# Performance work log

Measured on AMD Instinct MI355X. Metric: run time of the kernel, lower is better.

## Reference

```python
import jax, jax.numpy as jnp
import numpy as np

B, T, D, H = 8, 1024, 1024, 16
DH = D // H  # head dim = 64


def setup_inputs() -> dict:
    key = jax.random.key(0)
    ks = jax.random.split(key, 16)
    std_qk = np.sqrt(2.0 / (D + DH)).astype(np.float32)
    inp = {
        "query": jax.random.normal(ks[0], (B, T, D), jnp.float32),
        "key": jax.random.normal(ks[1], (B, T, D), jnp.float32),
        "value": jax.random.normal(ks[2], (B, T, D), jnp.float32),
        "spatial_encoding": jax.random.normal(ks[3], (B, T, T), jnp.float32),
        "edge_encoding": jax.random.normal(ks[4], (B, T, T), jnp.float32),
        "key_padding_mask": jax.random.bernoulli(ks[5], 0.1, (B, T)),  # True = masked key
        # Linear params stored as (in, out); y = x @ W + b (equivalent to torch x @ W.T + b)
        "Wq": jax.random.normal(ks[6], (D, D), jnp.float32) * std_qk,
        "bq": jnp.zeros((D,), jnp.float32),
        "Wk": jax.random.normal(ks[7], (D, D), jnp.float32) * std_qk,
        "bk": jnp.zeros((D,), jnp.float32),
        "Wv": jax.random.normal(ks[8], (D, D), jnp.float32) * std_qk,
        "bv": jnp.zeros((D,), jnp.float32),
        "Wo": jax.random.normal(ks[9], (D, D), jnp.float32),
        "bo": jnp.zeros((D,), jnp.float32),
    }
    return inp


def reference(query, key, value, spatial_encoding, edge_encoding, key_padding_mask,
              Wq, bq, Wk, bk, Wv, bv, Wo, bo):
    # QKV projections -> (B, H, T, DH)
    def proj(x, W, b):
        return (x @ W + b).reshape(B, T, H, DH).transpose(0, 2, 1, 3)

    q = proj(query, Wq, bq)
    k = proj(key, Wk, bk)
    v = proj(value, Wv, bv)

    # attention bias: spatial + edge, masked by key padding (broadcast over heads)
    attn_bias = (spatial_encoding + edge_encoding)[:, None, :, :]  # (B,1,T,T)
    neg_inf = jnp.float32(-jnp.inf)
    attn_bias = jnp.where(key_padding_mask[:, None, None, :], neg_inf, attn_bias)

    scale = 1.0 / np.sqrt(DH).astype(np.float32)
    scores = jnp.einsum('bhqd,bhkd->bhqk', q, k) * scale + attn_bias  # (B,H,T,T)
    attn = jax.nn.softmax(scores, axis=-1)
    out = jnp.einsum('bhqk,bhkd->bhqd', attn, v)  # (B,H,T,DH)
    out = out.transpose(0, 2, 1, 3).reshape(B, T, D)
    return out @ Wo + bo
```

## Files before the change

### kernel.cpp

```cpp
#include <hip/hip_runtime.h>
#include <hip/hip_bf16.h>

#define BB 8
#define TT 1024
#define DD 1024
#define HH 16
#define DH 64
#define QKVLD 3072

typedef __attribute__((ext_vector_type(8))) short short8;
typedef __attribute__((ext_vector_type(4))) float f32x4;

__device__ __forceinline__ unsigned short f2bf(float f) {
  unsigned int u = __builtin_bit_cast(unsigned int, f);
  unsigned int rounding = 0x7fffu + ((u >> 16) & 1u);
  u += rounding;
  return (unsigned short)(u >> 16);
}

__device__ __forceinline__ void gload16(const void* g, void* l) {
  __builtin_amdgcn_global_load_lds((const __attribute__((address_space(1))) void*)g,
                                   (__attribute__((address_space(3))) void*)l, 16, 0, 0);
}

__global__ __launch_bounds__(256) void convertT4_k(const float* __restrict__ w0,
                                                   const float* __restrict__ w1,
                                                   const float* __restrict__ w2,
                                                   const float* __restrict__ w3,
                                                   unsigned short* __restrict__ out) {
  int bx = blockIdx.x;
  int seg = bx >> 9;
  const float* in = seg == 0 ? w0 : seg == 1 ? w1 : seg == 2 ? w2 : w3;
  unsigned short* o = out + (size_t)seg * DD * DD;
  int g = (bx & 511) * 256 + threadIdx.x;
  int n = g & (DD - 1);
  int kb = (g >> 10) * 8;
  short8 v;
#pragma unroll
  for (int j = 0; j < 8; ++j) v[j] = (short)f2bf(in[(size_t)(kb + j) * DD + n]);
  *(short8*)(o + (size_t)n * DD + kb) = v;
}

__global__ __launch_bounds__(256) void gemm_qkv_k(const float* __restrict__ Aq,
                                                  const float* __restrict__ Ak,
                                                  const float* __restrict__ Av,
                                                  const unsigned short* __restrict__ Wt3,
                                                  const float* __restrict__ bq,
                                                  const float* __restrict__ bk,
                                                  const float* __restrict__ bv,
                                                  unsigned short* __restrict__ C) {
  __shared__ unsigned short Bs[128 * 64];
  __shared__ unsigned short As[128 * 72];
  const int tid = threadIdx.x, lane = tid & 63, w = tid >> 6;
  const int lo = lane & 15, hi = lane >> 4;
  const int wm = w >> 1, wn = w & 1;
  const int seg = blockIdx.x >> 3;
  const float* Ap = seg == 0 ? Aq : seg == 1 ? Ak : Av;
  const float* bias = seg == 0 ? bq : seg == 1 ? bk : bv;
  const int n0 = blockIdx.x * 128;
  const int m0 = blockIdx.y * 128;
  f32x4 acc[4][4] = {};
  int dmn[4], dmk[4];
#pragma unroll
  for (int i = 0; i < 4; ++i) {
    int d = i * 4096 + w * 1024 + lane * 16;
    int lz = d ^ (((d >> 7) & 7) << 4);
    dmn[i] = d >> 7;
    dmk[i] = (lz & 127) >> 1;
  }
  for (int k0 = 0; k0 < DD; k0 += 64) {
#pragma unroll
    for (int i = 0; i < 4; ++i)
      gload16(Wt3 + (size_t)(n0 + dmn[i]) * DD + k0 + dmk[i], &Bs[(i * 4096 + w * 1024) >> 1]);
#pragma unroll
    for (int it = 0; it < 4; ++it) {
      int c = tid + 256 * it;
      int r = c >> 3, cb = (c & 7) * 8;
      const float* src = Ap + (size_t)(m0 + r) * DD + k0 + cb;
      float4 v0 = *(const float4*)src;
      float4 v1 = *(const float4*)(src + 4);
      short8 sv;
      sv[0] = (short)f2bf(v0.x); sv[1] = (short)f2bf(v0.y);
      sv[2] = (short)f2bf(v0.z); sv[3] = (short)f2bf(v0.w);
      sv[4] = (short)f2bf(v1.x); sv[5] = (short)f2bf(v1.y);
      sv[6] = (short)f2bf(v1.z); sv[7] = (short)f2bf(v1.w);
      *(short8*)&As[r * 72 + cb] = sv;
    }
    __syncthreads();
#pragma unroll
    for (int s = 0; s < 2; ++s) {
      short8 af[4], bf[4];
#pragma unroll
      for (int mt = 0; mt < 4; ++mt)
        af[mt] = *(const short8*)&As[(wm * 64 + mt * 16 + lo) * 72 + s * 32 + hi * 8];
#pragma unroll
      for (int nt = 0; nt < 4; ++nt) {
        int nr = wn * 64 + nt * 16 + lo;
        int byte = (nr * 128 + s * 64 + hi * 16) ^ ((nr & 7) << 4);
        bf[nt] = *(const short8*)((const char*)Bs + byte);
      }
#pragma unroll
      for (int mt = 0; mt < 4; ++mt)
#pragma unroll
        for (int nt = 0; nt < 4; ++nt)
          acc[mt][nt] = __builtin_amdgcn_mfma_f32_16x16x32_bf16(af[mt], bf[nt], acc[mt][nt], 0, 0, 0);
    }
    __syncthreads();
  }
#pragma unroll
  for (int mt = 0; mt < 4; ++mt)
#pragma unroll
    for (int nt = 0; nt < 4; ++nt) {
      int cl = wn * 64 + nt * 16 + lo;
      float bvv = bias[(n0 & 1023) + cl];
      int col = n0 + cl;
#pragma unroll
      for (int r = 0; r < 4; ++r) {
        int row = m0 + wm * 64 + mt * 16 + hi * 4 + r;
        C[(size_t)row * QKVLD + col] = f2bf(acc[mt][nt][r] + bvv);
      }
    }
}

__global__ __launch_bounds__(256) void gemm_out_k(const unsigned short* __restrict__ Aobf,
                                                  const unsigned short* __restrict__ WoT,
                                                  const float* __restrict__ bo,
                                                  float* __restrict__ out) {
  __shared__ unsigned short Bs[128 * 64];
  __shared__ unsigned short As[128 * 64];
  const int tid = threadIdx.x, lane = tid & 63, w = tid >> 6;
  const int lo = lane & 15, hi = lane >> 4;
  const int wm = w >> 1, wn = w & 1;
  const int n0 = blockIdx.x * 128;
  const int m0 = blockIdx.y * 128;
  f32x4 acc[4][4] = {};
  int dmn[4], dmk[4];
#pragma unroll
  for (int i = 0; i < 4; ++i) {
    int d = i * 4096 + w * 1024 + lane * 16;
    int lz = d ^ (((d >> 7) & 7) << 4);
    dmn[i] = d >> 7;
    dmk[i] = (lz & 127) >> 1;
  }
  for (int k0 = 0; k0 < DD; k0 += 64) {
#pragma unroll
    for (int i = 0; i < 4; ++i) {
      gload16(WoT + (size_t)(n0 + dmn[i]) * DD + k0 + dmk[i], &Bs[(i * 4096 + w * 1024) >> 1]);
      gload16(Aobf + (size_t)(m0 + dmn[i]) * DD + k0 + dmk[i], &As[(i * 4096 + w * 1024) >> 1]);
    }
    __syncthreads();
#pragma unroll
    for (int s = 0; s < 2; ++s) {
      short8 af[4], bf[4];
#pragma unroll
      for (int mt = 0; mt < 4; ++mt) {
        int mr = wm * 64 + mt * 16 + lo;
        int byte = (mr * 128 + s * 64 + hi * 16) ^ ((mr & 7) << 4);
        af[mt] = *(const short8*)((const char*)As + byte);
      }
#pragma unroll
      for (int nt = 0; nt < 4; ++nt) {
        int nr = wn * 64 + nt * 16 + lo;
        int byte = (nr * 128 + s * 64 + hi * 16) ^ ((nr & 7) << 4);
        bf[nt] = *(const short8*)((const char*)Bs + byte);
      }
#pragma unroll
      for (int mt = 0; mt < 4; ++mt)
#pragma unroll
        for (int nt = 0; nt < 4; ++nt)
          acc[mt][nt] = __builtin_amdgcn_mfma_f32_16x16x32_bf16(af[mt], bf[nt], acc[mt][nt], 0, 0, 0);
    }
    __syncthreads();
  }
#pragma unroll
  for (int mt = 0; mt < 4; ++mt)
#pragma unroll
    for (int nt = 0; nt < 4; ++nt) {
      int col = n0 + wn * 64 + nt * 16 + lo;
      float bvv = bo[col];
#pragma unroll
      for (int r = 0; r < 4; ++r) {
        int row = m0 + wm * 64 + mt * 16 + hi * 4 + r;
        out[(size_t)row * DD + col] = acc[mt][nt][r] + bvv;
      }
    }
}

__global__ __launch_bounds__(256) void transpose_v_k(const unsigned short* __restrict__ QKV,
                                                     unsigned short* __restrict__ Vt) {
  __shared__ unsigned short tile[64][72];
  const int blk = blockIdx.x;
  const int t0 = (blk & 15) * 64;
  const int h = (blk >> 4) & 15;
  const int b = blk >> 8;
  const int tid = threadIdx.x;
#pragma unroll
  for (int it = 0; it < 2; ++it) {
    int c = tid + 256 * it;
    int r = c >> 3, d8 = (c & 7) * 8;
    short8 v = *(const short8*)(QKV + ((size_t)(b * TT + t0 + r)) * QKVLD + 2048 + h * DH + d8);
    *(short8*)&tile[r][d8] = v;
  }
  __syncthreads();
#pragma unroll
  for (int it = 0; it < 2; ++it) {
    int c = tid + 256 * it;
    int d = c >> 3, t8 = (c & 7) * 8;
    short8 o;
#pragma unroll
    for (int j = 0; j < 8; ++j) o[j] = (short)tile[t8 + j][d];
    *(short8*)(Vt + ((size_t)(b * HH + h) * DH + d) * TT + t0 + t8) = o;
  }
}

__global__ __launch_bounds__(256) void attn_k(const unsigned short* __restrict__ QKV,
                                              const unsigned short* __restrict__ Vt,
                                              const float* __restrict__ spat,
                                              const float* __restrict__ edge,
                                              const int* __restrict__ mask,
                                              unsigned short* __restrict__ Obf) {
  __shared__ unsigned short P[4][16][72];
  const int blk = blockIdx.x;
  const int qt = blk & 15;
  const int h = (blk >> 4) & 15;
  const int b = blk >> 8;
  const int tid = threadIdx.x;
  const int w = tid >> 6;
  const int lane = tid & 63;
  const int lo = lane & 15, hi = lane >> 4;
  const int q0 = qt * 64 + w * 16;

  const unsigned short* Qb = QKV + ((size_t)(b * TT + q0)) * QKVLD + h * DH;
  const unsigned short* Kb = QKV + (size_t)b * TT * QKVLD + 1024 + h * DH;
  const unsigned short* Vb = Vt + (size_t)(b * HH + h) * DH * TT;
  const float* Sp = spat + (size_t)b * TT * TT;
  const float* Ed = edge + (size_t)b * TT * TT;
  const int* Mk = mask + b * TT;

  short8 qf0 = *(const short8*)(Qb + (size_t)lo * QKVLD + hi * 8);
  short8 qf1 = *(const short8*)(Qb + (size_t)lo * QKVLD + 32 + hi * 8);

  float m[4], l[4];
  f32x4 acc[4] = {};
#pragma unroll
  for (int r = 0; r < 4; ++r) { m[r] = -INFINITY; l[r] = 0.f; }

  for (int k0 = 0; k0 < TT; k0 += 64) {
    short8 kf[8];
#pragma unroll
    for (int kt = 0; kt < 4; ++kt) {
      const unsigned short* kp = Kb + (size_t)(k0 + kt * 16 + lo) * QKVLD + hi * 8;
      kf[kt * 2] = *(const short8*)kp;
      kf[kt * 2 + 1] = *(const short8*)(kp + 32);
    }
    int mk[4];
#pragma unroll
    for (int kt = 0; kt < 4; ++kt) mk[kt] = Mk[k0 + kt * 16 + lo];

    f32x4 sc[4];
#pragma unroll
    for (int kt = 0; kt < 4; ++kt) {
      f32x4 z = {};
      z = __builtin_amdgcn_mfma_f32_16x16x32_bf16(qf0, kf[kt * 2], z, 0, 0, 0);
      sc[kt] = __builtin_amdgcn_mfma_f32_16x16x32_bf16(qf1, kf[kt * 2 + 1], z, 0, 0, 0);
    }

    float alpha[4];
#pragma unroll
    for (int r = 0; r < 4; ++r) {
      const size_t roff = (size_t)(q0 + hi * 4 + r) * TT + k0;
      const float* srow = Sp + roff;
      const float* erow = Ed + roff;
      float s[4];
#pragma unroll
      for (int j = 0; j < 4; ++j) {
        float bb = mk[j] ? -1e30f : (srow[j * 16 + lo] + erow[j * 16 + lo]);
        s[j] = sc[j][r] * 0.125f + bb;
      }
      float mx = fmaxf(fmaxf(s[0], s[1]), fmaxf(s[2], s[3]));
      mx = fmaxf(mx, __shfl_xor(mx, 1));
      mx = fmaxf(mx, __shfl_xor(mx, 2));
      mx = fmaxf(mx, __shfl_xor(mx, 4));
      mx = fmaxf(mx, __shfl_xor(mx, 8));
      float mn = fmaxf(m[r], mx);
      alpha[r] = __expf(m[r] - mn);
      m[r] = mn;
      float rs = 0.f;
#pragma unroll
      for (int j = 0; j < 4; ++j) {
        s[j] = __expf(s[j] - mn);
        rs += s[j];
        P[w][hi * 4 + r][j * 16 + lo] = f2bf(s[j]);
      }
      rs += __shfl_xor(rs, 1);
      rs += __shfl_xor(rs, 2);
      rs += __shfl_xor(rs, 4);
      rs += __shfl_xor(rs, 8);
      l[r] = l[r] * alpha[r] + rs;
    }
#pragma unroll
    for (int dt = 0; dt < 4; ++dt)
#pragma unroll
      for (int r = 0; r < 4; ++r) acc[dt][r] *= alpha[r];

#pragma unroll
    for (int kc = 0; kc < 2; ++kc) {
      short8 pf = *(const short8*)&P[w][lo][kc * 32 + hi * 8];
#pragma unroll
      for (int dt = 0; dt < 4; ++dt) {
        short8 vf = *(const short8*)(Vb + (size_t)(dt * 16 + lo) * TT + k0 + kc * 32 + hi * 8);
        acc[dt] = __builtin_amdgcn_mfma_f32_16x16x32_bf16(pf, vf, acc[dt], 0, 0, 0);
      }
    }
  }

  float rl[4];
#pragma unroll
  for (int r = 0; r < 4; ++r) rl[r] = 1.0f / l[r];
  unsigned short* Ob = Obf + ((size_t)b * TT + q0) * DD + h * DH;
#pragma unroll
  for (int dt = 0; dt < 4; ++dt)
#pragma unroll
    for (int r = 0; r < 4; ++r)
      Ob[(size_t)(hi * 4 + r) * DD + dt * 16 + lo] = f2bf(acc[dt][r] * rl[r]);
}

extern "C" void kernel_launch(void* const* d_in, const int* in_sizes, int n_in,
                              void* d_out, int out_size, void* d_ws, size_t ws_size,
                              hipStream_t stream) {
  const float* query = (const float*)d_in[0];
  const float* key   = (const float*)d_in[1];
  const float* value = (const float*)d_in[2];
  const float* spat  = (const float*)d_in[3];
  const float* edge  = (const float*)d_in[4];
  const int*   maskp = (const int*)d_in[5];
  const float* Wq = (const float*)d_in[6];  const float* bq = (const float*)d_in[7];
  const float* Wk = (const float*)d_in[8];  const float* bk = (const float*)d_in[9];
  const float* Wv = (const float*)d_in[10]; const float* bv = (const float*)d_in[11];
  const float* Wo = (const float*)d_in[12]; const float* bo = (const float*)d_in[13];
  float* out = (float*)d_out;

  const int M = BB * TT;
  unsigned short* WT3 = (unsigned short*)d_ws;
  unsigned short* WoT = WT3 + (size_t)3 * DD * DD;
  unsigned short* QKV = WoT + (size_t)DD * DD;
  unsigned short* Vt  = QKV + (size_t)M * QKVLD;
  unsigned short* Obf = Vt + (size_t)M * DD;

  convertT4_k<<<2048, 256, 0, stream>>>(Wq, Wk, Wv, Wo, WT3);

  gemm_qkv_k<<<dim3(24, M / 128), 256, 0, stream>>>(query, key, value, WT3, bq, bk, bv, QKV);

  transpose_v_k<<<BB * HH * (TT / 64), 256, 0, stream>>>(QKV, Vt);

  attn_k<<<BB * HH * (TT / 64), 256, 0, stream>>>(QKV, Vt, spat, edge, maskp, Obf);

  gemm_out_k<<<dim3(DD / 128, M / 128), 256, 0, stream>>>(Obf, WoT, bo, out);
}
```

Baseline: 746.4 us.

## Double-buffer bias tiles into LDS via async global loads in attention

The spatial and edge bias tiles are now prefetched one key block ahead into a double-buffered shared-memory area using direct global-to-LDS loads. The goal is to overlap the large fp32 bias reads with the MFMA and softmax work, instead of issuing scattered per-lane global loads inside the loop. The 1/sqrt(d) scale is also folded into Q once in bf16, which removes a multiply per score but rounds Q again. This adds 64KB of LDS per block, which may cut occupancy, and a block-wide barrier on every iteration.

```diff
diff --git a/kernel.cpp b/kernel.cpp
--- a/kernel.cpp
+++ b/kernel.cpp
@@ -16,6 +16,10 @@
   unsigned int rounding = 0x7fffu + ((u >> 16) & 1u);
   u += rounding;
   return (unsigned short)(u >> 16);
+}
+__device__ __forceinline__ float bf2f(unsigned short u) {
+  unsigned int x = ((unsigned int)u) << 16;
+  return __builtin_bit_cast(float, x);
 }
 
 __device__ __forceinline__ void gload16(const void* g, void* l) {
@@ -219,6 +223,7 @@
                                               const float* __restrict__ edge,
                                               const int* __restrict__ mask,
                                               unsigned short* __restrict__ Obf) {
+  __shared__ float SB[2][2][4][16][64];
   __shared__ unsigned short P[4][16][72];
   const int blk = blockIdx.x;
   const int qt = blk & 15;
@@ -233,19 +238,42 @@
   const unsigned short* Qb = QKV + ((size_t)(b * TT + q0)) * QKVLD + h * DH;
   const unsigned short* Kb = QKV + (size_t)b * TT * QKVLD + 1024 + h * DH;
   const unsigned short* Vb = Vt + (size_t)(b * HH + h) * DH * TT;
-  const float* Sp = spat + (size_t)b * TT * TT;
-  const float* Ed = edge + (size_t)b * TT * TT;
   const int* Mk = mask + b * TT;
-
-  short8 qf0 = *(const short8*)(Qb + (size_t)lo * QKVLD + hi * 8);
-  short8 qf1 = *(const short8*)(Qb + (size_t)lo * QKVLD + 32 + hi * 8);
+  const float* SpW = spat + (size_t)b * TT * TT + (size_t)(q0 + (lane >> 4)) * TT + (lane & 15) * 4;
+  const float* EdW = edge + (size_t)b * TT * TT + (size_t)(q0 + (lane >> 4)) * TT + (lane & 15) * 4;
+
+#define STAGE(bf, kk)                                              \
+  do {                                                             \
+    _Pragma("unroll") for (int i_ = 0; i_ < 4; ++i_) {             \
+      gload16(SpW + (size_t)i_ * 4 * TT + (kk), &SB[bf][0][w][i_ * 4][0]); \
+      gload16(EdW + (size_t)i_ * 4 * TT + (kk), &SB[bf][1][w][i_ * 4][0]); \
+    }                                                              \
+  } while (0)
+
+  short8 qf0, qf1;
+  {
+    short8 qr0 = *(const short8*)(Qb + (size_t)lo * QKVLD + hi * 8);
+    short8 qr1 = *(const short8*)(Qb + (size_t)lo * QKVLD + 32 + hi * 8);
+#pragma unroll
+    for (int j = 0; j < 8; ++j) {
+      qf0[j] = (short)f2bf(bf2f((unsigned short)qr0[j]) * 0.125f);
+      qf1[j] = (short)f2bf(bf2f((unsigned short)qr1[j]) * 0.125f);
+    }
+  }
 
   float m[4], l[4];
   f32x4 acc[4] = {};
 #pragma unroll
   for (int r = 0; r < 4; ++r) { m[r] = -INFINITY; l[r] = 0.f; }
 
-  for (int k0 = 0; k0 < TT; k0 += 64) {
+  STAGE(0, 0);
+  __syncthreads();
+
+  for (int t = 0; t < 16; ++t) {
+    const int k0 = t * 64;
+    const int cur = t & 1;
+    if (t < 15) STAGE(cur ^ 1, k0 + 64);
+
     short8 kf[8];
 #pragma unroll
     for (int kt = 0; kt < 4; ++kt) {
@@ -268,14 +296,13 @@
     float alpha[4];
 #pragma unroll
     for (int r = 0; r < 4; ++r) {
-      const size_t roff = (size_t)(q0 + hi * 4 + r) * TT + k0;
-      const float* srow = Sp + roff;
-      const float* erow = Ed + roff;
+      const float* srow = &SB[cur][0][w][hi * 4 + r][0];
+      const float* erow = &SB[cur][1][w][hi * 4 + r][0];
       float s[4];
 #pragma unroll
       for (int j = 0; j < 4; ++j) {
         float bb = mk[j] ? -1e30f : (srow[j * 16 + lo] + erow[j * 16 + lo]);
-        s[j] = sc[j][r] * 0.125f + bb;
+        s[j] = sc[j][r] + bb;
       }
       float mx = fmaxf(fmaxf(s[0], s[1]), fmaxf(s[2], s[3]));
       mx = fmaxf(mx, __shfl_xor(mx, 1));
@@ -312,7 +339,9 @@
         acc[dt] = __builtin_amdgcn_mfma_f32_16x16x32_bf16(pf, vf, acc[dt], 0, 0, 0);
       }
     }
-  }
+    __syncthreads();
+  }
+#undef STAGE
 
   float rl[4];
 #pragma unroll
```

After: 664.7 us. 10.9% less time.
